# Kernel optimization log

Hardware: AMD Instinct MI355X
Metric: run time of the kernel (lower is better)

Reference implementation:

```python
import jax, jax.numpy as jnp
import numpy as np

VX, VY = 0.2, 0.2
X_MIN, Y_MIN = -51.2, -51.2
Z_MIN, Z_MAX = -3.0, 3.0
GX, GY = 512, 512
NVOX = GX * GY
Z_CENTER = 0.0  # z_min + vz/2 with vz = 6.0
EPS = 1e-3  # BN1d default eps in mmdet3d PFNLayer


def _voxel_ids(pts):
    # pts: [B, N, 3] -> integer pillar coords and flat ids
    ix = jnp.clip(jnp.floor((pts[..., 0] - X_MIN) / VX).astype(jnp.int32), 0, GX - 1)
    iy = jnp.clip(jnp.floor((pts[..., 1] - Y_MIN) / VY).astype(jnp.int32), 0, GY - 1)
    return ix, iy, ix * GY + iy


def _segment_mean(vals, ids, n):
    # vals: [N, C], ids: [N] -> [n, C] mean per segment (0 for empty)
    s = jax.ops.segment_sum(vals, ids, num_segments=n)
    c = jax.ops.segment_sum(jnp.ones(vals.shape[0], vals.dtype), ids, num_segments=n)
    return s / jnp.maximum(c, 1.0)[:, None]


def _pillar_grid(pts, W, gamma, beta, mean, var):
    # DynamicPillarFeatureNet: point aug -> linear -> BN(eval) -> relu -> scatter-mean
    ix, iy, vid = _voxel_ids(pts)  # [B, N]
    fdt = pts.dtype
    # cluster center: per-voxel mean of xyz, gathered back to points
    cluster_mean = jax.vmap(lambda p, i: _segment_mean(p, i, NVOX)[i])(pts, vid)  # [B,N,3]
    center = jnp.stack([
        (ix.astype(fdt) + 0.5) * VX + X_MIN,
        (iy.astype(fdt) + 0.5) * VY + Y_MIN,
        jnp.full(ix.shape, Z_CENTER, dtype=fdt),
    ], axis=-1)  # [B,N,3]
    f = jnp.concatenate([pts, pts - cluster_mean, pts - center], axis=-1)  # [B,N,9]
    h = jnp.einsum('bnf,fc->bnc', f, W)  # Linear(9 -> C), no bias (BN follows)
    h = jax.nn.relu(gamma * (h - mean) * jax.lax.rsqrt(var + EPS) + beta)  # [B,N,C]
    # scatter mean per pillar -> dense grid (zeros where empty)
    grid = jax.vmap(lambda v, i: _segment_mean(v, i, NVOX))(h, vid)  # [B, NVOX, C]
    return grid


def setup_inputs() -> dict:
    key = jax.random.key(0)
    k0, k1, kw = jax.random.split(key, 3)
    B, N, C = 2, 100000, 64
    lo = jnp.array([X_MIN, Y_MIN, Z_MIN], jnp.float32)
    hi = jnp.array([-X_MIN, -Y_MIN, Z_MAX], jnp.float32)
    pc0s = jax.random.uniform(k0, (B, N, 3), jnp.float32) * (hi - lo) + lo
    pc1s = jax.random.uniform(k1, (B, N, 3), jnp.float32) * (hi - lo) + lo
    W = jax.random.normal(kw, (9, C), jnp.float32) * (1.0 / np.sqrt(9.0))
    return {
        'pc0s': pc0s, 'pc1s': pc1s, 'W': W,
        'bn_gamma': jnp.ones((C,), jnp.float32),
        'bn_beta': jnp.zeros((C,), jnp.float32),
        'bn_mean': jnp.zeros((C,), jnp.float32),
        'bn_var': jnp.ones((C,), jnp.float32),
    }


def reference(pc0s, pc1s, W, bn_gamma, bn_beta, bn_mean, bn_var):
    g0 = _pillar_grid(pc0s, W, bn_gamma, bn_beta, bn_mean, bn_var)
    g1 = _pillar_grid(pc1s, W, bn_gamma, bn_beta, bn_mean, bn_var)
    # sparse_pc1 - sparse_pc0, coalesced: identical to dense grid difference
    diff = (g1 - g0).reshape(pc0s.shape[0], GX, GY, -1)  # [B, GX, GY, C]
    return diff
```

## Files before the change

### kernel.cpp

```cpp
#include <hip/hip_runtime.h>

#define VXC 0.2f
#define VYC 0.2f
#define XMINC -51.2f
#define YMINC -51.2f
#define GXD 512
#define GYD 512
#define NVOXD (GXD * GYD)
#define BN_EPS 1e-3f

__global__ void init_and_precompute(int* __restrict__ cnt, int nzero4,
                                    const float* __restrict__ W,
                                    const float* __restrict__ gamma,
                                    const float* __restrict__ beta,
                                    const float* __restrict__ mean,
                                    const float* __restrict__ var,
                                    float* __restrict__ P) {
    int nzero_blocks = (nzero4 + 255) / 256;
    if ((int)blockIdx.x < nzero_blocks) {
        int i = blockIdx.x * 256 + threadIdx.x;
        if (i < nzero4) ((int4*)cnt)[i] = make_int4(0, 0, 0, 0);
        return;
    }
    int c = threadIdx.x;
    if (c >= 64) return;
    float scale = gamma[c] * (1.0f / sqrtf(var[c] + BN_EPS));
    float w0 = W[0*64+c], w1 = W[1*64+c], w2 = W[2*64+c];
    float w3 = W[3*64+c], w4 = W[4*64+c], w5 = W[5*64+c];
    float w6 = W[6*64+c], w7 = W[7*64+c], w8 = W[8*64+c];
    P[0*64+c] = (w0 + w3 + w6) * scale;
    P[1*64+c] = (w1 + w4 + w7) * scale;
    P[2*64+c] = (w2 + w5 + w8) * scale;
    P[3*64+c] = w3 * scale;
    P[4*64+c] = w4 * scale;
    P[5*64+c] = w5 * scale;
    P[6*64+c] = w6 * scale;
    P[7*64+c] = w7 * scale;
    P[8*64+c] = beta[c] - mean[c] * scale;
}

__global__ void bin_points(const float* __restrict__ pc0, const float* __restrict__ pc1,
                           int* __restrict__ cnt, uint4* __restrict__ pk4,
                           int B, int N) {
    int i = blockIdx.x * blockDim.x + threadIdx.x;
    int per4 = (B * N) >> 2;
    if (i >= 2 * per4) return;
    int cloud = (i >= per4) ? 1 : 0;
    int i2 = i - cloud * per4;
    int b = i2 / (N >> 2);
    const float4* p4 = (const float4*)(cloud ? pc1 : pc0) + (size_t)i2 * 3;
    float4 q0 = p4[0], q1 = p4[1], q2 = p4[2];
    float xs[4] = {q0.x, q0.w, q1.z, q2.y};
    float ys[4] = {q0.y, q1.x, q1.w, q2.z};
    int vbase = (cloud * B + b) * NVOXD;
    unsigned r[4];
    #pragma unroll
    for (int k = 0; k < 4; ++k) {
        int ix = (int)floorf((xs[k] - XMINC) / VXC); ix = min(max(ix, 0), GXD - 1);
        int iy = (int)floorf((ys[k] - YMINC) / VYC); iy = min(max(iy, 0), GYD - 1);
        int hidx = vbase + ix * GYD + iy;
        int pos = atomicAdd(cnt + hidx, 1);
        r[k] = ((unsigned)hidx << 8) | (unsigned)pos;
    }
    pk4[i] = make_uint4(r[0], r[1], r[2], r[3]);
}

__global__ void scan_block(const int* __restrict__ in, int* __restrict__ out,
                           int* __restrict__ bsums) {
    int tid = threadIdx.x;
    size_t base = (size_t)blockIdx.x * 1024;
    int4 v = ((const int4*)(in + base))[tid];
    int t0 = v.x, t1 = t0 + v.y, t2 = t1 + v.z, t3 = t2 + v.w;
    __shared__ int lds[256];
    lds[tid] = t3;
    __syncthreads();
    for (int d = 1; d < 256; d <<= 1) {
        int t = (tid >= d) ? lds[tid - d] : 0;
        __syncthreads();
        lds[tid] += t;
        __syncthreads();
    }
    int excl = lds[tid] - t3;
    if (tid == 255) bsums[blockIdx.x] = lds[255];
    ((int4*)(out + base))[tid] = make_int4(excl, excl + t0, excl + t1, excl + t2);
}

__global__ void add_bases(int* __restrict__ off, const int* __restrict__ bases,
                          int n4, int total) {
    int i = blockIdx.x * blockDim.x + threadIdx.x;
    if (i >= n4) return;
    int4 v = ((int4*)off)[i];
    int b = bases[i >> 8];
    v.x += b; v.y += b; v.z += b; v.w += b;
    ((int4*)off)[i] = v;
    if (i == 0) off[n4 * 4] = total;
}

__global__ void scatter_csr(const float* __restrict__ pc0, const float* __restrict__ pc1,
                            const int* __restrict__ off, const uint4* __restrict__ pk4,
                            float4* __restrict__ csr, int B, int N) {
    int i = blockIdx.x * blockDim.x + threadIdx.x;
    int per4 = (B * N) >> 2;
    if (i >= 2 * per4) return;
    int cloud = (i >= per4) ? 1 : 0;
    int i2 = i - cloud * per4;
    const float4* p4 = (const float4*)(cloud ? pc1 : pc0) + (size_t)i2 * 3;
    float4 q0 = p4[0], q1 = p4[1], q2 = p4[2];
    uint4 pkv = pk4[i];
    float xs[4] = {q0.x, q0.w, q1.z, q2.y};
    float ys[4] = {q0.y, q1.x, q1.w, q2.z};
    float zs[4] = {q0.z, q1.y, q2.x, q2.w};
    unsigned pr[4] = {pkv.x, pkv.y, pkv.z, pkv.w};
    #pragma unroll
    for (int k = 0; k < 4; ++k) {
        int o = off[pr[k] >> 8] + (int)(pr[k] & 255u);
        csr[o] = make_float4(xs[k], ys[k], zs[k], 0.0f);
    }
}

__global__ __launch_bounds__(256)
void gather(const float4* __restrict__ csr, const int* __restrict__ off,
            const float* __restrict__ P, float* __restrict__ out, int B) {
    int g = blockIdx.x * blockDim.x + threadIdx.x;
    int c = g & 63;
    int w = g >> 6;
    int noct = (B * NVOXD) >> 3;
    if (w >= noct) return;

    float A   = P[0*64+c], Bw  = P[1*64+c], Cw  = P[2*64+c];
    float w3s = P[3*64+c], w4s = P[4*64+c], w5s = P[5*64+c];
    float w6s = P[6*64+c], w7s = P[7*64+c], offc = P[8*64+c];
    float A1 = A - w3s, B1 = Bw - w4s, C1 = Cw - w5s;
    int base1 = B * NVOXD;
    int bv0 = w << 3;

    int4 a0  = *(const int4*)(off + bv0);
    int4 a0b = *(const int4*)(off + bv0 + 4);
    int4 a1  = *(const int4*)(off + base1 + bv0);
    int4 a1b = *(const int4*)(off + base1 + bv0 + 4);
    int o0[9] = {a0.x, a0.y, a0.z, a0.w, a0b.x, a0b.y, a0b.z, a0b.w,
                 off[bv0 + 8]};
    int o1[9] = {a1.x, a1.y, a1.z, a1.w, a1b.x, a1b.y, a1b.z, a1b.w,
                 off[base1 + bv0 + 8]};

    #pragma unroll
    for (int q = 0; q < 8; ++q) {
        int bv = bv0 + q;
        int s0 = o0[q], e0 = o0[q + 1];
        int s1 = o1[q], e1 = o1[q + 1];
        float res = 0.0f;
        if (e0 > s0 || e1 > s1) {
            int v = bv & (NVOXD - 1);
            int ix = v >> 9, iy = v & 511;
            float cx = ((float)ix + 0.5f) * VXC + XMINC;
            float cy = ((float)iy + 0.5f) * VYC + YMINC;
            float basef = offc - cx * w6s - cy * w7s;
            int n0 = e0 - s0;
            if (n0 == 1) {
                float4 pt = csr[s0];
                res -= fmaxf(pt.x * A1 + pt.y * B1 + pt.z * C1 + basef, 0.0f);
            } else if (n0 > 1) {
                float sx = 0.0f, sy = 0.0f, sz = 0.0f;
                for (int j = s0; j < e0; ++j) {
                    float4 pt = csr[j];
                    sx += pt.x; sy += pt.y; sz += pt.z;
                }
                float inv = 1.0f / (float)n0;
                float cbias = basef - (sx * w3s + sy * w4s + sz * w5s) * inv;
                float hsum = 0.0f;
                for (int j = s0; j < e0; ++j) {
                    float4 pt = csr[j];
                    hsum += fmaxf(pt.x * A + pt.y * Bw + pt.z * Cw + cbias, 0.0f);
                }
                res -= hsum * inv;
            }
            int n1 = e1 - s1;
            if (n1 == 1) {
                float4 pt = csr[s1];
                res += fmaxf(pt.x * A1 + pt.y * B1 + pt.z * C1 + basef, 0.0f);
            } else if (n1 > 1) {
                float sx = 0.0f, sy = 0.0f, sz = 0.0f;
                for (int j = s1; j < e1; ++j) {
                    float4 pt = csr[j];
                    sx += pt.x; sy += pt.y; sz += pt.z;
                }
                float inv = 1.0f / (float)n1;
                float cbias = basef - (sx * w3s + sy * w4s + sz * w5s) * inv;
                float hsum = 0.0f;
                for (int j = s1; j < e1; ++j) {
                    float4 pt = csr[j];
                    hsum += fmaxf(pt.x * A + pt.y * Bw + pt.z * Cw + cbias, 0.0f);
                }
                res += hsum * inv;
            }
        }
        __builtin_nontemporal_store(res, out + ((size_t)bv << 6) + c);
    }
}

extern "C" void kernel_launch(void* const* d_in, const int* in_sizes, int n_in,
                              void* d_out, int out_size, void* d_ws, size_t ws_size,
                              hipStream_t stream) {
    const float* pc0   = (const float*)d_in[0];
    const float* pc1   = (const float*)d_in[1];
    const float* Wm    = (const float*)d_in[2];
    const float* gamma = (const float*)d_in[3];
    const float* beta  = (const float*)d_in[4];
    const float* mean  = (const float*)d_in[5];
    const float* var   = (const float*)d_in[6];
    float* out = (float*)d_out;

    int B = out_size / (NVOXD * 64);
    int N = in_sizes[0] / (3 * B);
    int npts = 2 * B * N;
    int n = 2 * B * NVOXD;
    int nblocks_scan = n / 1024;

    float4* csr   = (float4*)d_ws;
    int* off      = (int*)(csr + npts + 4);
    int* aux      = off + n + 4;
    int* aux2     = aux + nblocks_scan;
    unsigned* pk  = (unsigned*)(aux2 + nblocks_scan);
    float* P      = (float*)(pk + npts);

    int nzero4 = n / 4;
    int nzero_blocks = (nzero4 + 255) / 256;
    init_and_precompute<<<nzero_blocks + 1, 256, 0, stream>>>(
        off, nzero4, Wm, gamma, beta, mean, var, P);

    int nq = npts / 4;
    int g1 = (nq + 255) / 256;
    bin_points<<<g1, 256, 0, stream>>>(pc0, pc1, off, (uint4*)pk, B, N);

    scan_block<<<nblocks_scan, 256, 0, stream>>>(off, off, aux);
    scan_block<<<1, 256, 0, stream>>>(aux, aux, aux2);
    add_bases<<<(n / 4 + 255) / 256, 256, 0, stream>>>(off, aux, n / 4, npts);

    scatter_csr<<<g1, 256, 0, stream>>>(pc0, pc1, off, (const uint4*)pk, csr, B, N);

    long long total_thr = ((long long)B * NVOXD >> 3) * 64;
    int g4 = (int)((total_thr + 255) / 256);
    gather<<<g4, 256, 0, stream>>>(csr, off, P, out, B);
}
```

Measured before the change: 215.0 us.

## Replace three-pass scan with one-pass block scan plus consumer-side base fixup

```diff
diff --git a/kernel.cpp b/kernel.cpp
--- a/kernel.cpp
+++ b/kernel.cpp
@@ -8,6 +8,7 @@
 #define GYD 512
 #define NVOXD (GXD * GYD)
 #define BN_EPS 1e-3f
+#define SUPER 4096
 
 __global__ void init_and_precompute(int* __restrict__ cnt, int nzero4,
                                     const float* __restrict__ W,
@@ -65,14 +66,21 @@
     pk4[i] = make_uint4(r[0], r[1], r[2], r[3]);
 }
 
-__global__ void scan_block(const int* __restrict__ in, int* __restrict__ out,
-                           int* __restrict__ bsums) {
+__global__ __launch_bounds__(256)
+void scan_super(int* __restrict__ off, int* __restrict__ bsums) {
     int tid = threadIdx.x;
-    size_t base = (size_t)blockIdx.x * 1024;
-    int4 v = ((const int4*)(in + base))[tid];
-    int t0 = v.x, t1 = t0 + v.y, t2 = t1 + v.z, t3 = t2 + v.w;
+    size_t base = (size_t)blockIdx.x * SUPER + (size_t)tid * 16;
+    int4 a = ((const int4*)(off + base))[0];
+    int4 bq = ((const int4*)(off + base))[1];
+    int4 cq = ((const int4*)(off + base))[2];
+    int4 dq = ((const int4*)(off + base))[3];
+    int s[16] = {a.x,a.y,a.z,a.w, bq.x,bq.y,bq.z,bq.w,
+                 cq.x,cq.y,cq.z,cq.w, dq.x,dq.y,dq.z,dq.w};
+    int tot = 0;
+    #pragma unroll
+    for (int k = 0; k < 16; ++k) tot += s[k];
     __shared__ int lds[256];
-    lds[tid] = t3;
+    lds[tid] = tot;
     __syncthreads();
     for (int d = 1; d < 256; d <<= 1) {
         int t = (tid >= d) ? lds[tid - d] : 0;
@@ -80,25 +88,41 @@
         lds[tid] += t;
         __syncthreads();
     }
-    int excl = lds[tid] - t3;
+    int run = lds[tid] - tot;
     if (tid == 255) bsums[blockIdx.x] = lds[255];
-    ((int4*)(out + base))[tid] = make_int4(excl, excl + t0, excl + t1, excl + t2);
-}
-
-__global__ void add_bases(int* __restrict__ off, const int* __restrict__ bases,
-                          int n4, int total) {
-    int i = blockIdx.x * blockDim.x + threadIdx.x;
-    if (i >= n4) return;
-    int4 v = ((int4*)off)[i];
-    int b = bases[i >> 8];
-    v.x += b; v.y += b; v.z += b; v.w += b;
-    ((int4*)off)[i] = v;
-    if (i == 0) off[n4 * 4] = total;
-}
-
-__global__ void scatter_csr(const float* __restrict__ pc0, const float* __restrict__ pc1,
-                            const int* __restrict__ off, const uint4* __restrict__ pk4,
-                            float4* __restrict__ csr, int B, int N) {
+    int o[16];
+    #pragma unroll
+    for (int k = 0; k < 16; ++k) { o[k] = run; run += s[k]; }
+    ((int4*)(off + base))[0] = make_int4(o[0], o[1], o[2], o[3]);
+    ((int4*)(off + base))[1] = make_int4(o[4], o[5], o[6], o[7]);
+    ((int4*)(off + base))[2] = make_int4(o[8], o[9], o[10], o[11]);
+    ((int4*)(off + base))[3] = make_int4(o[12], o[13], o[14], o[15]);
+}
+
+__device__ __forceinline__ void scan_bases(const int* __restrict__ bsums, int* sb) {
+    int tid = threadIdx.x;
+    int v = bsums[tid];
+    sb[tid] = v;
+    __syncthreads();
+    for (int d = 1; d < 256; d <<= 1) {
+        int t = (tid >= d) ? sb[tid - d] : 0;
+        __syncthreads();
+        sb[tid] += t;
+        __syncthreads();
+    }
+    int incl = sb[tid];
+    __syncthreads();
+    sb[tid] = incl - v;
+    __syncthreads();
+}
+
+__global__ __launch_bounds__(256)
+void scatter_csr(const float* __restrict__ pc0, const float* __restrict__ pc1,
+                 const int* __restrict__ off, const int* __restrict__ bsums,
+                 const uint4* __restrict__ pk4, float4* __restrict__ csr,
+                 int B, int N) {
+    __shared__ int sb[256];
+    scan_bases(bsums, sb);
     int i = blockIdx.x * blockDim.x + threadIdx.x;
     int per4 = (B * N) >> 2;
     if (i >= 2 * per4) return;
@@ -113,14 +137,18 @@
     unsigned pr[4] = {pkv.x, pkv.y, pkv.z, pkv.w};
     #pragma unroll
     for (int k = 0; k < 4; ++k) {
-        int o = off[pr[k] >> 8] + (int)(pr[k] & 255u);
+        int bin = (int)(pr[k] >> 8);
+        int o = off[bin] + sb[bin >> 12] + (int)(pr[k] & 255u);
         csr[o] = make_float4(xs[k], ys[k], zs[k], 0.0f);
     }
 }
 
 __global__ __launch_bounds__(256)
 void gather(const float4* __restrict__ csr, const int* __restrict__ off,
-            const float* __restrict__ P, float* __restrict__ out, int B) {
+            const int* __restrict__ bsums, const float* __restrict__ P,
+            float* __restrict__ out, int B, int n, int npts) {
+    __shared__ int sb[256];
+    scan_bases(bsums, sb);
     int g = blockIdx.x * blockDim.x + threadIdx.x;
     int c = g & 63;
     int w = g >> 6;
@@ -138,16 +166,25 @@
     int4 a0b = *(const int4*)(off + bv0 + 4);
     int4 a1  = *(const int4*)(off + base1 + bv0);
     int4 a1b = *(const int4*)(off + base1 + bv0 + 4);
-    int o0[9] = {a0.x, a0.y, a0.z, a0.w, a0b.x, a0b.y, a0b.z, a0b.w,
+    int r0[9] = {a0.x, a0.y, a0.z, a0.w, a0b.x, a0b.y, a0b.z, a0b.w,
                  off[bv0 + 8]};
-    int o1[9] = {a1.x, a1.y, a1.z, a1.w, a1b.x, a1b.y, a1b.z, a1b.w,
-                 off[base1 + bv0 + 8]};
+    int last1 = (base1 + bv0 + 8 < n) ? off[base1 + bv0 + 8] : 0;
+    int r1[9] = {a1.x, a1.y, a1.z, a1.w, a1b.x, a1b.y, a1b.z, a1b.w, last1};
+
+    int f0[9], f1[9];
+    #pragma unroll
+    for (int k = 0; k < 9; ++k) {
+        int idx0 = bv0 + k;
+        f0[k] = r0[k] + sb[idx0 >> 12];
+        int idx1 = base1 + bv0 + k;
+        f1[k] = (idx1 == n) ? npts : r1[k] + sb[idx1 >> 12];
+    }
 
     #pragma unroll
     for (int q = 0; q < 8; ++q) {
         int bv = bv0 + q;
-        int s0 = o0[q], e0 = o0[q + 1];
-        int s1 = o1[q], e1 = o1[q + 1];
+        int s0 = f0[q], e0 = f0[q + 1];
+        int s1 = f1[q], e1 = f1[q + 1];
         float res = 0.0f;
         if (e0 > s0 || e1 > s1) {
             int v = bv & (NVOXD - 1);
@@ -214,13 +251,12 @@
     int N = in_sizes[0] / (3 * B);
     int npts = 2 * B * N;
     int n = 2 * B * NVOXD;
-    int nblocks_scan = n / 1024;
+    int nsuper = n / SUPER;
 
     float4* csr   = (float4*)d_ws;
     int* off      = (int*)(csr + npts + 4);
-    int* aux      = off + n + 4;
-    int* aux2     = aux + nblocks_scan;
-    unsigned* pk  = (unsigned*)(aux2 + nblocks_scan);
+    int* bsums    = off + n;
+    unsigned* pk  = (unsigned*)(bsums + 256);
     float* P      = (float*)(pk + npts);
 
     int nzero4 = n / 4;
@@ -232,13 +268,12 @@
     int g1 = (nq + 255) / 256;
     bin_points<<<g1, 256, 0, stream>>>(pc0, pc1, off, (uint4*)pk, B, N);
 
-    scan_block<<<nblocks_scan, 256, 0, stream>>>(off, off, aux);
-    scan_block<<<1, 256, 0, stream>>>(aux, aux, aux2);
-    add_bases<<<(n / 4 + 255) / 256, 256, 0, stream>>>(off, aux, n / 4, npts);
-
-    scatter_csr<<<g1, 256, 0, stream>>>(pc0, pc1, off, (const uint4*)pk, csr, B, N);
+    scan_super<<<nsuper, 256, 0, stream>>>(off, bsums);
+
+    scatter_csr<<<g1, 256, 0, stream>>>(pc0, pc1, off, bsums, (const uint4*)pk,
+                                        csr, B, N);
 
     long long total_thr = ((long long)B * NVOXD >> 3) * 64;
-    int g4 = (int)((total_thr + 255) / 256);
-    gather<<<g4, 256, 0, stream>>>(csr, off, P, out, B);
-}
+    int g2 = (int)((total_thr + 255) / 256);
+    gather<<<g2, 256, 0, stream>>>(csr, off, bsums, P, out, B, n, npts);
+}
```

Measured after the change: 222.4 us. 1.03x slower.

## Fuse binning, scan, scatter and gather into one persistent kernel with grid barriers

Applied to the files above, without the earlier changes.

```diff
diff --git a/kernel.cpp b/kernel.cpp
--- a/kernel.cpp
+++ b/kernel.cpp
@@ -8,6 +8,7 @@
 #define GYD 512
 #define NVOXD (GXD * GYD)
 #define BN_EPS 1e-3f
+#define NBLK 1024
 
 __global__ void init_and_precompute(int* __restrict__ cnt, int nzero4,
                                     const float* __restrict__ W,
@@ -39,162 +40,179 @@
     P[8*64+c] = beta[c] - mean[c] * scale;
 }
 
-__global__ void bin_points(const float* __restrict__ pc0, const float* __restrict__ pc1,
-                           int* __restrict__ cnt, uint4* __restrict__ pk4,
-                           int B, int N) {
-    int i = blockIdx.x * blockDim.x + threadIdx.x;
+__device__ __forceinline__ void gbar(int* bar) {
+    __syncthreads();
+    if (threadIdx.x == 0) {
+        __hip_atomic_fetch_add(bar, 1, __ATOMIC_RELEASE, __HIP_MEMORY_SCOPE_AGENT);
+        while (__hip_atomic_load(bar, __ATOMIC_RELAXED, __HIP_MEMORY_SCOPE_AGENT) < NBLK)
+            __builtin_amdgcn_s_sleep(2);
+        int x = __hip_atomic_load(bar, __ATOMIC_ACQUIRE, __HIP_MEMORY_SCOPE_AGENT);
+        (void)x;
+    }
+    __syncthreads();
+}
+
+__global__ __launch_bounds__(256, 4)
+void mega(const float* __restrict__ pc0, const float* __restrict__ pc1,
+          int* __restrict__ off, int* __restrict__ bar,
+          int* __restrict__ bsums, int* __restrict__ aux,
+          float4* __restrict__ csr, const float* __restrict__ P,
+          float* __restrict__ out, int B, int N, int npts, int n) {
+    int tid = threadIdx.x;
+    int gi = blockIdx.x * 256 + tid;
+    int nq2 = npts >> 2;
     int per4 = (B * N) >> 2;
-    if (i >= 2 * per4) return;
-    int cloud = (i >= per4) ? 1 : 0;
-    int i2 = i - cloud * per4;
-    int b = i2 / (N >> 2);
-    const float4* p4 = (const float4*)(cloud ? pc1 : pc0) + (size_t)i2 * 3;
-    float4 q0 = p4[0], q1 = p4[1], q2 = p4[2];
-    float xs[4] = {q0.x, q0.w, q1.z, q2.y};
-    float ys[4] = {q0.y, q1.x, q1.w, q2.z};
-    int vbase = (cloud * B + b) * NVOXD;
-    unsigned r[4];
-    #pragma unroll
-    for (int k = 0; k < 4; ++k) {
-        int ix = (int)floorf((xs[k] - XMINC) / VXC); ix = min(max(ix, 0), GXD - 1);
-        int iy = (int)floorf((ys[k] - YMINC) / VYC); iy = min(max(iy, 0), GYD - 1);
-        int hidx = vbase + ix * GYD + iy;
-        int pos = atomicAdd(cnt + hidx, 1);
-        r[k] = ((unsigned)hidx << 8) | (unsigned)pos;
-    }
-    pk4[i] = make_uint4(r[0], r[1], r[2], r[3]);
-}
-
-__global__ void scan_block(const int* __restrict__ in, int* __restrict__ out,
-                           int* __restrict__ bsums) {
-    int tid = threadIdx.x;
-    size_t base = (size_t)blockIdx.x * 1024;
-    int4 v = ((const int4*)(in + base))[tid];
-    int t0 = v.x, t1 = t0 + v.y, t2 = t1 + v.z, t3 = t2 + v.w;
+
+    float4 q0, q1, q2; unsigned r[4];
+    bool active = gi < nq2;
+    if (active) {
+        int cloud = (gi >= per4) ? 1 : 0;
+        int i2 = gi - cloud * per4;
+        int b = i2 / (N >> 2);
+        const float4* p4 = (const float4*)(cloud ? pc1 : pc0) + (size_t)i2 * 3;
+        q0 = p4[0]; q1 = p4[1]; q2 = p4[2];
+        float xs[4] = {q0.x, q0.w, q1.z, q2.y};
+        float ys[4] = {q0.y, q1.x, q1.w, q2.z};
+        int vbase = (cloud * B + b) * NVOXD;
+        #pragma unroll
+        for (int k = 0; k < 4; ++k) {
+            int ix = (int)floorf((xs[k] - XMINC) / VXC); ix = min(max(ix, 0), GXD - 1);
+            int iy = (int)floorf((ys[k] - YMINC) / VYC); iy = min(max(iy, 0), GYD - 1);
+            int hidx = vbase + ix * GYD + iy;
+            int pos = atomicAdd(off + hidx, 1);
+            r[k] = ((unsigned)hidx << 8) | (unsigned)pos;
+        }
+    }
+    gbar(bar + 0);
+
     __shared__ int lds[256];
-    lds[tid] = t3;
-    __syncthreads();
-    for (int d = 1; d < 256; d <<= 1) {
-        int t = (tid >= d) ? lds[tid - d] : 0;
+    {
+        size_t base = (size_t)blockIdx.x * 1024 + (size_t)tid * 4;
+        int4 v = *(const int4*)(off + base);
+        int t0 = v.x, t1 = t0 + v.y, t2 = t1 + v.z, t3 = t2 + v.w;
+        lds[tid] = t3;
         __syncthreads();
-        lds[tid] += t;
+        for (int d = 1; d < 256; d <<= 1) {
+            int t = (tid >= d) ? lds[tid - d] : 0;
+            __syncthreads();
+            lds[tid] += t;
+            __syncthreads();
+        }
+        int excl = lds[tid] - t3;
+        if (tid == 255) bsums[blockIdx.x] = lds[255];
+        *(int4*)(off + base) = make_int4(excl, excl + t0, excl + t1, excl + t2);
+    }
+    gbar(bar + 1);
+
+    if (blockIdx.x == 0) {
+        int4 v = *(const int4*)(bsums + tid * 4);
+        int t0 = v.x, t1 = t0 + v.y, t2 = t1 + v.z, t3 = t2 + v.w;
+        lds[tid] = t3;
         __syncthreads();
-    }
-    int excl = lds[tid] - t3;
-    if (tid == 255) bsums[blockIdx.x] = lds[255];
-    ((int4*)(out + base))[tid] = make_int4(excl, excl + t0, excl + t1, excl + t2);
-}
-
-__global__ void add_bases(int* __restrict__ off, const int* __restrict__ bases,
-                          int n4, int total) {
-    int i = blockIdx.x * blockDim.x + threadIdx.x;
-    if (i >= n4) return;
-    int4 v = ((int4*)off)[i];
-    int b = bases[i >> 8];
-    v.x += b; v.y += b; v.z += b; v.w += b;
-    ((int4*)off)[i] = v;
-    if (i == 0) off[n4 * 4] = total;
-}
-
-__global__ void scatter_csr(const float* __restrict__ pc0, const float* __restrict__ pc1,
-                            const int* __restrict__ off, const uint4* __restrict__ pk4,
-                            float4* __restrict__ csr, int B, int N) {
-    int i = blockIdx.x * blockDim.x + threadIdx.x;
-    int per4 = (B * N) >> 2;
-    if (i >= 2 * per4) return;
-    int cloud = (i >= per4) ? 1 : 0;
-    int i2 = i - cloud * per4;
-    const float4* p4 = (const float4*)(cloud ? pc1 : pc0) + (size_t)i2 * 3;
-    float4 q0 = p4[0], q1 = p4[1], q2 = p4[2];
-    uint4 pkv = pk4[i];
-    float xs[4] = {q0.x, q0.w, q1.z, q2.y};
-    float ys[4] = {q0.y, q1.x, q1.w, q2.z};
-    float zs[4] = {q0.z, q1.y, q2.x, q2.w};
-    unsigned pr[4] = {pkv.x, pkv.y, pkv.z, pkv.w};
-    #pragma unroll
-    for (int k = 0; k < 4; ++k) {
-        int o = off[pr[k] >> 8] + (int)(pr[k] & 255u);
-        csr[o] = make_float4(xs[k], ys[k], zs[k], 0.0f);
-    }
-}
-
-__global__ __launch_bounds__(256)
-void gather(const float4* __restrict__ csr, const int* __restrict__ off,
-            const float* __restrict__ P, float* __restrict__ out, int B) {
-    int g = blockIdx.x * blockDim.x + threadIdx.x;
-    int c = g & 63;
-    int w = g >> 6;
-    int noct = (B * NVOXD) >> 3;
-    if (w >= noct) return;
-
+        for (int d = 1; d < 256; d <<= 1) {
+            int t = (tid >= d) ? lds[tid - d] : 0;
+            __syncthreads();
+            lds[tid] += t;
+            __syncthreads();
+        }
+        int excl = lds[tid] - t3;
+        *(int4*)(aux + tid * 4) = make_int4(excl, excl + t0, excl + t1, excl + t2);
+    }
+    gbar(bar + 2);
+
+    if (active) {
+        float xs[4] = {q0.x, q0.w, q1.z, q2.y};
+        float ys[4] = {q0.y, q1.x, q1.w, q2.z};
+        float zs[4] = {q0.z, q1.y, q2.x, q2.w};
+        #pragma unroll
+        for (int k = 0; k < 4; ++k) {
+            int bin = (int)(r[k] >> 8);
+            int o = off[bin] + aux[bin >> 10] + (int)(r[k] & 255u);
+            csr[o] = make_float4(xs[k], ys[k], zs[k], 0.0f);
+        }
+    }
+    gbar(bar + 3);
+
+    int c = tid & 63;
     float A   = P[0*64+c], Bw  = P[1*64+c], Cw  = P[2*64+c];
     float w3s = P[3*64+c], w4s = P[4*64+c], w5s = P[5*64+c];
     float w6s = P[6*64+c], w7s = P[7*64+c], offc = P[8*64+c];
     float A1 = A - w3s, B1 = Bw - w4s, C1 = Cw - w5s;
     int base1 = B * NVOXD;
-    int bv0 = w << 3;
-
-    int4 a0  = *(const int4*)(off + bv0);
-    int4 a0b = *(const int4*)(off + bv0 + 4);
-    int4 a1  = *(const int4*)(off + base1 + bv0);
-    int4 a1b = *(const int4*)(off + base1 + bv0 + 4);
-    int o0[9] = {a0.x, a0.y, a0.z, a0.w, a0b.x, a0b.y, a0b.z, a0b.w,
-                 off[bv0 + 8]};
-    int o1[9] = {a1.x, a1.y, a1.z, a1.w, a1b.x, a1b.y, a1b.z, a1b.w,
-                 off[base1 + bv0 + 8]};
-
-    #pragma unroll
-    for (int q = 0; q < 8; ++q) {
-        int bv = bv0 + q;
-        int s0 = o0[q], e0 = o0[q + 1];
-        int s1 = o1[q], e1 = o1[q + 1];
-        float res = 0.0f;
-        if (e0 > s0 || e1 > s1) {
-            int v = bv & (NVOXD - 1);
-            int ix = v >> 9, iy = v & 511;
-            float cx = ((float)ix + 0.5f) * VXC + XMINC;
-            float cy = ((float)iy + 0.5f) * VYC + YMINC;
-            float basef = offc - cx * w6s - cy * w7s;
-            int n0 = e0 - s0;
-            if (n0 == 1) {
-                float4 pt = csr[s0];
-                res -= fmaxf(pt.x * A1 + pt.y * B1 + pt.z * C1 + basef, 0.0f);
-            } else if (n0 > 1) {
-                float sx = 0.0f, sy = 0.0f, sz = 0.0f;
-                for (int j = s0; j < e0; ++j) {
-                    float4 pt = csr[j];
-                    sx += pt.x; sy += pt.y; sz += pt.z;
+    int noct = base1 >> 3;
+    int gw = gi >> 6;
+
+    for (int w = gw; w < noct; w += NBLK * 4) {
+        int bv0 = w << 3;
+        int4 a0  = *(const int4*)(off + bv0);
+        int4 a0b = *(const int4*)(off + bv0 + 4);
+        int4 a1  = *(const int4*)(off + base1 + bv0);
+        int4 a1b = *(const int4*)(off + base1 + bv0 + 4);
+        int r0[9] = {a0.x, a0.y, a0.z, a0.w, a0b.x, a0b.y, a0b.z, a0b.w,
+                     off[bv0 + 8]};
+        int idx1_last = base1 + bv0 + 8;
+        int r1[9] = {a1.x, a1.y, a1.z, a1.w, a1b.x, a1b.y, a1b.z, a1b.w,
+                     (idx1_last < n) ? off[idx1_last] : 0};
+        int f0[9], f1[9];
+        #pragma unroll
+        for (int k = 0; k < 9; ++k) {
+            f0[k] = r0[k] + aux[(bv0 + k) >> 10];
+            int idx1 = base1 + bv0 + k;
+            f1[k] = (idx1 == n) ? npts : r1[k] + aux[idx1 >> 10];
+        }
+        #pragma unroll
+        for (int q = 0; q < 8; ++q) {
+            int bv = bv0 + q;
+            int s0 = f0[q], e0 = f0[q + 1];
+            int s1 = f1[q], e1 = f1[q + 1];
+            float res = 0.0f;
+            if (e0 > s0 || e1 > s1) {
+                int v = bv & (NVOXD - 1);
+                int ix = v >> 9, iy = v & 511;
+                float cx = ((float)ix + 0.5f) * VXC + XMINC;
+                float cy = ((float)iy + 0.5f) * VYC + YMINC;
+                float basef = offc - cx * w6s - cy * w7s;
+                int n0 = e0 - s0;
+                if (n0 == 1) {
+                    float4 pt = csr[s0];
+                    res -= fmaxf(pt.x * A1 + pt.y * B1 + pt.z * C1 + basef, 0.0f);
+                } else if (n0 > 1) {
+                    float sx = 0.0f, sy = 0.0f, sz = 0.0f;
+                    for (int j = s0; j < e0; ++j) {
+                        float4 pt = csr[j];
+                        sx += pt.x; sy += pt.y; sz += pt.z;
+                    }
+                    float inv = 1.0f / (float)n0;
+                    float cbias = basef - (sx * w3s + sy * w4s + sz * w5s) * inv;
+                    float hsum = 0.0f;
+                    for (int j = s0; j < e0; ++j) {
+                        float4 pt = csr[j];
+                        hsum += fmaxf(pt.x * A + pt.y * Bw + pt.z * Cw + cbias, 0.0f);
+                    }
+                    res -= hsum * inv;
                 }
-                float inv = 1.0f / (float)n0;
-                float cbias = basef - (sx * w3s + sy * w4s + sz * w5s) * inv;
-                float hsum = 0.0f;
-                for (int j = s0; j < e0; ++j) {
-                    float4 pt = csr[j];
-                    hsum += fmaxf(pt.x * A + pt.y * Bw + pt.z * Cw + cbias, 0.0f);
+                int n1 = e1 - s1;
+                if (n1 == 1) {
+                    float4 pt = csr[s1];
+                    res += fmaxf(pt.x * A1 + pt.y * B1 + pt.z * C1 + basef, 0.0f);
+                } else if (n1 > 1) {
+                    float sx = 0.0f, sy = 0.0f, sz = 0.0f;
+                    for (int j = s1; j < e1; ++j) {
+                        float4 pt = csr[j];
+                        sx += pt.x; sy += pt.y; sz += pt.z;
+                    }
+                    float inv = 1.0f / (float)n1;
+                    float cbias = basef - (sx * w3s + sy * w4s + sz * w5s) * inv;
+                    float hsum = 0.0f;
+                    for (int j = s1; j < e1; ++j) {
+                        float4 pt = csr[j];
+                        hsum += fmaxf(pt.x * A + pt.y * Bw + pt.z * Cw + cbias, 0.0f);
+                    }
+                    res += hsum * inv;
                 }
-                res -= hsum * inv;
             }
-            int n1 = e1 - s1;
-            if (n1 == 1) {
-                float4 pt = csr[s1];
-                res += fmaxf(pt.x * A1 + pt.y * B1 + pt.z * C1 + basef, 0.0f);
-            } else if (n1 > 1) {
-                float sx = 0.0f, sy = 0.0f, sz = 0.0f;
-                for (int j = s1; j < e1; ++j) {
-                    float4 pt = csr[j];
-                    sx += pt.x; sy += pt.y; sz += pt.z;
-                }
-                float inv = 1.0f / (float)n1;
-                float cbias = basef - (sx * w3s + sy * w4s + sz * w5s) * inv;
-                float hsum = 0.0f;
-                for (int j = s1; j < e1; ++j) {
-                    float4 pt = csr[j];
-                    hsum += fmaxf(pt.x * A + pt.y * Bw + pt.z * Cw + cbias, 0.0f);
-                }
-                res += hsum * inv;
-            }
-        }
-        __builtin_nontemporal_store(res, out + ((size_t)bv << 6) + c);
+            __builtin_nontemporal_store(res, out + ((size_t)bv << 6) + c);
+        }
     }
 }
 
@@ -214,31 +232,19 @@
     int N = in_sizes[0] / (3 * B);
     int npts = 2 * B * N;
     int n = 2 * B * NVOXD;
-    int nblocks_scan = n / 1024;
 
     float4* csr   = (float4*)d_ws;
     int* off      = (int*)(csr + npts + 4);
-    int* aux      = off + n + 4;
-    int* aux2     = aux + nblocks_scan;
-    unsigned* pk  = (unsigned*)(aux2 + nblocks_scan);
-    float* P      = (float*)(pk + npts);
-
-    int nzero4 = n / 4;
+    int* bar      = off + n + 4;
+    int* bsums    = bar + 8;
+    int* aux      = bsums + NBLK;
+    float* P      = (float*)(aux + NBLK);
+
+    int nzero4 = n / 4 + 3;
     int nzero_blocks = (nzero4 + 255) / 256;
     init_and_precompute<<<nzero_blocks + 1, 256, 0, stream>>>(
         off, nzero4, Wm, gamma, beta, mean, var, P);
 
-    int nq = npts / 4;
-    int g1 = (nq + 255) / 256;
-    bin_points<<<g1, 256, 0, stream>>>(pc0, pc1, off, (uint4*)pk, B, N);
-
-    scan_block<<<nblocks_scan, 256, 0, stream>>>(off, off, aux);
-    scan_block<<<1, 256, 0, stream>>>(aux, aux, aux2);
-    add_bases<<<(n / 4 + 255) / 256, 256, 0, stream>>>(off, aux, n / 4, npts);
-
-    scatter_csr<<<g1, 256, 0, stream>>>(pc0, pc1, off, (const uint4*)pk, csr, B, N);
-
-    long long total_thr = ((long long)B * NVOXD >> 3) * 64;
-    int g4 = (int)((total_thr + 255) / 256);
-    gather<<<g4, 256, 0, stream>>>(csr, off, P, out, B);
-}
+    mega<<<NBLK, 256, 0, stream>>>(pc0, pc1, off, bar, bsums, aux, csr, P, out,
+                                   B, N, npts, n);
+}
```

After: 571.6 us. 2.66x slower.

## Drop add_bases pass and vectorize gather to four channels per lane

Applied to the files above, without the earlier changes.

```diff
diff --git a/kernel.cpp b/kernel.cpp
--- a/kernel.cpp
+++ b/kernel.cpp
@@ -8,6 +8,8 @@
 #define GYD 512
 #define NVOXD (GXD * GYD)
 #define BN_EPS 1e-3f
+
+typedef float vfloat4 __attribute__((ext_vector_type(4)));
 
 __global__ void init_and_precompute(int* __restrict__ cnt, int nzero4,
                                     const float* __restrict__ W,
@@ -85,20 +87,10 @@
     ((int4*)(out + base))[tid] = make_int4(excl, excl + t0, excl + t1, excl + t2);
 }
 
-__global__ void add_bases(int* __restrict__ off, const int* __restrict__ bases,
-                          int n4, int total) {
-    int i = blockIdx.x * blockDim.x + threadIdx.x;
-    if (i >= n4) return;
-    int4 v = ((int4*)off)[i];
-    int b = bases[i >> 8];
-    v.x += b; v.y += b; v.z += b; v.w += b;
-    ((int4*)off)[i] = v;
-    if (i == 0) off[n4 * 4] = total;
-}
-
 __global__ void scatter_csr(const float* __restrict__ pc0, const float* __restrict__ pc1,
-                            const int* __restrict__ off, const uint4* __restrict__ pk4,
-                            float4* __restrict__ csr, int B, int N) {
+                            const int* __restrict__ off, const int* __restrict__ bases,
+                            const uint4* __restrict__ pk4, float4* __restrict__ csr,
+                            int B, int N) {
     int i = blockIdx.x * blockDim.x + threadIdx.x;
     int per4 = (B * N) >> 2;
     if (i >= 2 * per4) return;
@@ -113,52 +105,57 @@
     unsigned pr[4] = {pkv.x, pkv.y, pkv.z, pkv.w};
     #pragma unroll
     for (int k = 0; k < 4; ++k) {
-        int o = off[pr[k] >> 8] + (int)(pr[k] & 255u);
+        int bin = (int)(pr[k] >> 8);
+        int o = off[bin] + bases[bin >> 10] + (int)(pr[k] & 255u);
         csr[o] = make_float4(xs[k], ys[k], zs[k], 0.0f);
     }
 }
 
 __global__ __launch_bounds__(256)
 void gather(const float4* __restrict__ csr, const int* __restrict__ off,
-            const float* __restrict__ P, float* __restrict__ out, int B) {
+            const int* __restrict__ bases, const float* __restrict__ P,
+            float* __restrict__ out, int B, int n, int npts) {
     int g = blockIdx.x * blockDim.x + threadIdx.x;
-    int c = g & 63;
+    int lane = g & 63;
     int w = g >> 6;
     int noct = (B * NVOXD) >> 3;
     if (w >= noct) return;
-
-    float A   = P[0*64+c], Bw  = P[1*64+c], Cw  = P[2*64+c];
-    float w3s = P[3*64+c], w4s = P[4*64+c], w5s = P[5*64+c];
-    float w6s = P[6*64+c], w7s = P[7*64+c], offc = P[8*64+c];
-    float A1 = A - w3s, B1 = Bw - w4s, C1 = Cw - w5s;
+    int sub = lane >> 4;
+    int ch = (lane & 15) << 2;
+
+    float A[4], Bw[4], Cw[4], w3s[4], w4s[4], w5s[4], w6s[4], w7s[4], offc[4];
+    #pragma unroll
+    for (int k = 0; k < 4; ++k) {
+        A[k]    = P[0*64+ch+k]; Bw[k]  = P[1*64+ch+k]; Cw[k]  = P[2*64+ch+k];
+        w3s[k]  = P[3*64+ch+k]; w4s[k] = P[4*64+ch+k]; w5s[k] = P[5*64+ch+k];
+        w6s[k]  = P[6*64+ch+k]; w7s[k] = P[7*64+ch+k]; offc[k]= P[8*64+ch+k];
+    }
     int base1 = B * NVOXD;
-    int bv0 = w << 3;
-
-    int4 a0  = *(const int4*)(off + bv0);
-    int4 a0b = *(const int4*)(off + bv0 + 4);
-    int4 a1  = *(const int4*)(off + base1 + bv0);
-    int4 a1b = *(const int4*)(off + base1 + bv0 + 4);
-    int o0[9] = {a0.x, a0.y, a0.z, a0.w, a0b.x, a0b.y, a0b.z, a0b.w,
-                 off[bv0 + 8]};
-    int o1[9] = {a1.x, a1.y, a1.z, a1.w, a1b.x, a1b.y, a1b.z, a1b.w,
-                 off[base1 + bv0 + 8]};
-
-    #pragma unroll
-    for (int q = 0; q < 8; ++q) {
-        int bv = bv0 + q;
-        int s0 = o0[q], e0 = o0[q + 1];
-        int s1 = o1[q], e1 = o1[q + 1];
-        float res = 0.0f;
-        if (e0 > s0 || e1 > s1) {
+
+    #pragma unroll
+    for (int s = 0; s < 2; ++s) {
+        int bv = (w << 3) + s * 4 + sub;
+        int i0 = bv, i0e = bv + 1;
+        int i1 = base1 + bv, i1e = i1 + 1;
+        int s0 = off[i0]  + bases[i0 >> 10];
+        int e0 = off[i0e] + bases[i0e >> 10];
+        int s1 = off[i1]  + bases[i1 >> 10];
+        int e1 = (i1e == n) ? npts : off[i1e] + bases[i1e >> 10];
+        float r[4] = {0.0f, 0.0f, 0.0f, 0.0f};
+        int n0 = e0 - s0, n1 = e1 - s1;
+        if (n0 > 0 || n1 > 0) {
             int v = bv & (NVOXD - 1);
-            int ix = v >> 9, iy = v & 511;
-            float cx = ((float)ix + 0.5f) * VXC + XMINC;
-            float cy = ((float)iy + 0.5f) * VYC + YMINC;
-            float basef = offc - cx * w6s - cy * w7s;
-            int n0 = e0 - s0;
+            float cx = ((float)(v >> 9) + 0.5f) * VXC + XMINC;
+            float cy = ((float)(v & 511) + 0.5f) * VYC + YMINC;
+            float bf[4];
+            #pragma unroll
+            for (int k = 0; k < 4; ++k) bf[k] = offc[k] - cx * w6s[k] - cy * w7s[k];
             if (n0 == 1) {
                 float4 pt = csr[s0];
-                res -= fmaxf(pt.x * A1 + pt.y * B1 + pt.z * C1 + basef, 0.0f);
+                #pragma unroll
+                for (int k = 0; k < 4; ++k)
+                    r[k] -= fmaxf(pt.x * (A[k] - w3s[k]) + pt.y * (Bw[k] - w4s[k])
+                                  + pt.z * (Cw[k] - w5s[k]) + bf[k], 0.0f);
             } else if (n0 > 1) {
                 float sx = 0.0f, sy = 0.0f, sz = 0.0f;
                 for (int j = s0; j < e0; ++j) {
@@ -166,18 +163,25 @@
                     sx += pt.x; sy += pt.y; sz += pt.z;
                 }
                 float inv = 1.0f / (float)n0;
-                float cbias = basef - (sx * w3s + sy * w4s + sz * w5s) * inv;
-                float hsum = 0.0f;
+                float cb[4], h[4] = {0.0f, 0.0f, 0.0f, 0.0f};
+                #pragma unroll
+                for (int k = 0; k < 4; ++k)
+                    cb[k] = bf[k] - (sx * w3s[k] + sy * w4s[k] + sz * w5s[k]) * inv;
                 for (int j = s0; j < e0; ++j) {
                     float4 pt = csr[j];
-                    hsum += fmaxf(pt.x * A + pt.y * Bw + pt.z * Cw + cbias, 0.0f);
-                }
-                res -= hsum * inv;
+                    #pragma unroll
+                    for (int k = 0; k < 4; ++k)
+                        h[k] += fmaxf(pt.x * A[k] + pt.y * Bw[k] + pt.z * Cw[k] + cb[k], 0.0f);
+                }
+                #pragma unroll
+                for (int k = 0; k < 4; ++k) r[k] -= h[k] * inv;
             }
-            int n1 = e1 - s1;
             if (n1 == 1) {
                 float4 pt = csr[s1];
-                res += fmaxf(pt.x * A1 + pt.y * B1 + pt.z * C1 + basef, 0.0f);
+                #pragma unroll
+                for (int k = 0; k < 4; ++k)
+                    r[k] += fmaxf(pt.x * (A[k] - w3s[k]) + pt.y * (Bw[k] - w4s[k])
+                                  + pt.z * (Cw[k] - w5s[k]) + bf[k], 0.0f);
             } else if (n1 > 1) {
                 float sx = 0.0f, sy = 0.0f, sz = 0.0f;
                 for (int j = s1; j < e1; ++j) {
@@ -185,16 +189,22 @@
                     sx += pt.x; sy += pt.y; sz += pt.z;
                 }
                 float inv = 1.0f / (float)n1;
-                float cbias = basef - (sx * w3s + sy * w4s + sz * w5s) * inv;
-                float hsum = 0.0f;
+                float cb[4], h[4] = {0.0f, 0.0f, 0.0f, 0.0f};
+                #pragma unroll
+                for (int k = 0; k < 4; ++k)
+                    cb[k] = bf[k] - (sx * w3s[k] + sy * w4s[k] + sz * w5s[k]) * inv;
                 for (int j = s1; j < e1; ++j) {
                     float4 pt = csr[j];
-                    hsum += fmaxf(pt.x * A + pt.y * Bw + pt.z * Cw + cbias, 0.0f);
-                }
-                res += hsum * inv;
+                    #pragma unroll
+                    for (int k = 0; k < 4; ++k)
+                        h[k] += fmaxf(pt.x * A[k] + pt.y * Bw[k] + pt.z * Cw[k] + cb[k], 0.0f);
+                }
+                #pragma unroll
+                for (int k = 0; k < 4; ++k) r[k] += h[k] * inv;
             }
         }
-        __builtin_nontemporal_store(res, out + ((size_t)bv << 6) + c);
+        vfloat4 v4 = {r[0], r[1], r[2], r[3]};
+        __builtin_nontemporal_store(v4, (vfloat4*)(out + ((size_t)bv << 6) + ch));
     }
 }
 
@@ -218,9 +228,9 @@
 
     float4* csr   = (float4*)d_ws;
     int* off      = (int*)(csr + npts + 4);
-    int* aux      = off + n + 4;
-    int* aux2     = aux + nblocks_scan;
-    unsigned* pk  = (unsigned*)(aux2 + nblocks_scan);
+    int* bsums    = off + n;
+    int* scratch  = bsums + nblocks_scan;
+    unsigned* pk  = (unsigned*)(scratch + 4);
     float* P      = (float*)(pk + npts);
 
     int nzero4 = n / 4;
@@ -232,13 +242,13 @@
     int g1 = (nq + 255) / 256;
     bin_points<<<g1, 256, 0, stream>>>(pc0, pc1, off, (uint4*)pk, B, N);
 
-    scan_block<<<nblocks_scan, 256, 0, stream>>>(off, off, aux);
-    scan_block<<<1, 256, 0, stream>>>(aux, aux, aux2);
-    add_bases<<<(n / 4 + 255) / 256, 256, 0, stream>>>(off, aux, n / 4, npts);
-
-    scatter_csr<<<g1, 256, 0, stream>>>(pc0, pc1, off, (const uint4*)pk, csr, B, N);
+    scan_block<<<nblocks_scan, 256, 0, stream>>>(off, off, bsums);
+    scan_block<<<1, 256, 0, stream>>>(bsums, bsums, scratch);
+
+    scatter_csr<<<g1, 256, 0, stream>>>(pc0, pc1, off, bsums, (const uint4*)pk,
+                                        csr, B, N);
 
     long long total_thr = ((long long)B * NVOXD >> 3) * 64;
-    int g4 = (int)((total_thr + 255) / 256);
-    gather<<<g4, 256, 0, stream>>>(csr, off, P, out, B);
-}
+    int g2 = (int)((total_thr + 255) / 256);
+    gather<<<g2, 256, 0, stream>>>(csr, off, bsums, P, out, B, n, npts);
+}
```

Result: slower. 225.8 us (+5.0%).
